# Kernel tuning notes

Hardware: AMD Instinct MI355X
Metric: run time of the kernel (lower is better)

Reference implementation:

```python
import jax, jax.numpy as jnp
import numpy as np

B, N, D, H = 8, 2048, 256, 8
HD = D // H  # head_dim = 32
LN_EPS = 1e-5


def setup_inputs() -> dict:
    key = jax.random.key(0)
    ks = jax.random.split(key, 8)
    x = jax.random.normal(ks[0], (B, N, D), dtype=jnp.float32)
    # dense 0/1 adjacency with guaranteed self-loops (avoids all -inf softmax rows)
    adj = jax.random.randint(ks[1], (B, N, N), 0, 2, dtype=jnp.int32)
    adj = jnp.maximum(adj, jnp.eye(N, dtype=jnp.int32)[None, :, :])
    s = 0.02
    Wq = jax.random.normal(ks[2], (D, D), dtype=jnp.float32) * s
    Wk = jax.random.normal(ks[3], (D, D), dtype=jnp.float32) * s
    Wv = jax.random.normal(ks[4], (D, D), dtype=jnp.float32) * s
    Wo = jax.random.normal(ks[5], (D, D), dtype=jnp.float32) * s
    zeros = jnp.zeros((D,), dtype=jnp.float32)
    return {
        "x": x, "adjacency": adj,
        "Wq": Wq, "bq": zeros, "Wk": Wk, "bk": zeros,
        "Wv": Wv, "bv": zeros, "Wo": Wo, "bo": zeros,
        "gamma": jnp.ones((D,), dtype=jnp.float32), "beta": zeros,
    }


def reference(x, adjacency, Wq, bq, Wk, bk, Wv, bv, Wo, bo, gamma, beta):
    b, n, d = x.shape
    q = (x @ Wq + bq).reshape(b, n, H, HD)
    k = (x @ Wk + bk).reshape(b, n, H, HD)
    v = (x @ Wv + bv).reshape(b, n, H, HD)
    # scores: [B, N(query), M(key), H]
    scores = jnp.einsum('bnhd,bmhd->bnmh', q, k) / jnp.sqrt(jnp.float32(HD))
    mask = (adjacency == 0)[..., None]  # [B,N,M,1] broadcasts over heads
    scores = jnp.where(mask, -jnp.inf, scores)
    weights = jax.nn.softmax(scores, axis=2)  # softmax over key axis m
    # dropout is identity in eval mode
    attended = jnp.einsum('bnmh,bmhd->bnhd', weights, v).reshape(b, n, d)
    out = attended @ Wo + bo
    out = out + x  # residual (output.shape == x.shape since input_dim == output_dim)
    mu = jnp.mean(out, axis=-1, keepdims=True)
    var = jnp.mean(jnp.square(out - mu), axis=-1, keepdims=True)
    return (out - mu) * jax.lax.rsqrt(var + LN_EPS) * gamma + beta
```

## Files before the change

### kernel.cpp

```cpp
#include <hip/hip_runtime.h>
#include <hip/hip_bf16.h>
#include <cstdint>
#include <cstddef>

#define B_ 8
#define N_ 2048
#define D_ 256
#define H_ 8
#define HD_ 32
#define LN_EPS 1e-5f
#define QSCALE 0.25506275f

typedef __attribute__((ext_vector_type(8))) short short8;
typedef __attribute__((ext_vector_type(4))) float f32x4;
typedef __attribute__((ext_vector_type(16))) float f32x16;

static __device__ __forceinline__ float exp2v(float x) {
#if __has_builtin(__builtin_amdgcn_exp2f)
    return __builtin_amdgcn_exp2f(x);
#else
    float r;
    asm("v_exp_f32 %0, %1" : "=v"(r) : "v"(x));
    return r;
#endif
}

static __device__ __forceinline__ unsigned short f2bf(float f) {
    union { float f; unsigned int u; } v; v.f = f;
    unsigned int r = v.u + 0x7fffu + ((v.u >> 16) & 1u);
    return (unsigned short)(r >> 16);
}

static __device__ __forceinline__ unsigned int cvtpk(float lo, float hi) {
    unsigned int d;
    asm("v_cvt_pk_bf16_f32 %0, %1, %2" : "=v"(d) : "v"(lo), "v"(hi));
    return d;
}

__global__ __launch_bounds__(256) void k_prep_w(const float* __restrict__ w0, const float* __restrict__ w1,
                                                const float* __restrict__ w2, const float* __restrict__ w3,
                                                unsigned short* __restrict__ wt) {
    int c = blockIdx.x, mat = blockIdx.y, k = threadIdx.x;
    const float* w = (mat == 0) ? w0 : (mat == 1) ? w1 : (mat == 2) ? w2 : w3;
    wt[((size_t)(mat * 256 + c)) * 256 + k] = f2bf(w[k * 256 + c]);
}

__global__ __launch_bounds__(512) void k_maskF(const int* __restrict__ adj,
                                               unsigned int* __restrict__ mbgT2) {
    __shared__ unsigned int bits[64][66];
    int tid = threadIdx.x, lane = tid & 63, wv = tid >> 6;
    int b = blockIdx.x >> 5, rg = blockIdx.x & 31;

    const int* base = adj + ((size_t)(b * N_ + rg * 64 + wv * 8)) * N_ + lane;
#pragma unroll 1
    for (int i = 0; i < 8; ++i) {
        const int* prow = base + (size_t)i * N_;
#pragma unroll
        for (int half = 0; half < 2; ++half) {
            int v[16];
#pragma unroll
            for (int j = 0; j < 16; ++j)
                v[j] = prow[half * 1024 + j * 64];
            __builtin_amdgcn_sched_barrier(0);
#pragma unroll
            for (int j = 0; j < 16; ++j) {
                unsigned long long m = __ballot(v[j] != 0);
                if (lane == 0)
                    *reinterpret_cast<unsigned long long*>(&bits[wv * 8 + i][half * 32 + 2 * j]) = m;
            }
        }
    }
    __syncthreads();

    int h = lane >> 5, l31 = lane & 31;
    const unsigned int M[5] = {0x0000FFFFu, 0x00FF00FFu, 0x0F0F0F0Fu, 0x33333333u, 0x55555555u};
#pragma unroll
    for (int j = 0; j < 8; ++j) {
        int kw = wv * 8 + j;
        unsigned int w = bits[lane][kw];
#pragma unroll
        for (int si = 0; si < 5; ++si) {
            int s = 16 >> si;
            unsigned int m = M[si];
            unsigned int t = (unsigned int)__shfl_xor((int)w, s, 64);
            unsigned int a = (w & m) | ((t & m) << s);
            unsigned int c = (w & ~m) | ((t >> s) & m);
            w = (lane & s) ? c : a;
        }
        int k = kw * 32 + l31;
        int kp = (k & ~7) | ((k & 3) << 1) | ((k >> 2) & 1);
        mbgT2[((size_t)(b * 64 + rg * 2 + h)) * 2048 + kp] = w;
    }
}

__global__ __launch_bounds__(256) void k_qkv(const float* __restrict__ x,
                                             const unsigned short* __restrict__ wt,
                                             const float* __restrict__ bq, const float* __restrict__ bk,
                                             const float* __restrict__ bv,
                                             unsigned short* __restrict__ Qts, unsigned short* __restrict__ Ks,
                                             unsigned short* __restrict__ Vs) {
    int mat = blockIdx.y;
    int lane = threadIdx.x & 63;
    int wv = threadIdx.x >> 6;
    int row0 = blockIdx.x * 64 + wv * 16;
    int l15 = lane & 15, lg = lane >> 4;
    const float* bias = (mat == 0) ? bq : (mat == 1) ? bk : bv;
    const float qs = (mat == 0) ? QSCALE : 1.0f;
    const unsigned short* wm = wt + (size_t)mat * 65536;

    short8 af[8];
    const float* xrow = x + (size_t)(row0 + l15) * 256 + lg * 8;
#pragma unroll
    for (int kk = 0; kk < 8; ++kk) {
        float4 a = *reinterpret_cast<const float4*>(xrow + kk * 32);
        float4 b = *reinterpret_cast<const float4*>(xrow + kk * 32 + 4);
        union { short8 s8; unsigned int u[4]; } t;
        t.u[0] = cvtpk(a.x, a.y); t.u[1] = cvtpk(a.z, a.w);
        t.u[2] = cvtpk(b.x, b.y); t.u[3] = cvtpk(b.z, b.w);
        af[kk] = t.s8;
    }

    int b = row0 >> 11;
    int nbase = (row0 & 2047) + lg * 4;

    if (mat < 2) {
        unsigned short* dst = (mat == 0) ? Qts : Ks;
        int n = (row0 & 2047) + l15;
        for (int ci = 0; ci < 16; ++ci) {
            const unsigned short* wrow = wm + (size_t)(ci * 16 + l15) * 256 + lg * 8;
            f32x4 acc = {0.f, 0.f, 0.f, 0.f};
#pragma unroll
            for (int kk = 0; kk < 8; ++kk) {
                short8 bfg = *reinterpret_cast<const short8*>(wrow + kk * 32);
                acc = __builtin_amdgcn_mfma_f32_16x16x32_bf16(bfg, af[kk], acc, 0, 0, 0);
            }
            int col0 = ci * 16 + lg * 4;
            float4 b4 = *reinterpret_cast<const float4*>(bias + col0);
            int h = col0 >> 5;
            int hd0 = col0 & 31;
            size_t off = (size_t)(b * 8 + h) * 65536 + (size_t)(n >> 5) * 1024
                       + (size_t)(hd0 >> 4) * 512
                       + (size_t)((((hd0 >> 3) & 1) * 32 + (n & 31))) * 8 + (hd0 & 7);
            ushort4 o;
            o.x = f2bf((acc[0] + b4.x) * qs); o.y = f2bf((acc[1] + b4.y) * qs);
            o.z = f2bf((acc[2] + b4.z) * qs); o.w = f2bf((acc[3] + b4.w) * qs);
            *reinterpret_cast<ushort4*>(dst + off) = o;
        }
    } else {
        for (int ci = 0; ci < 16; ++ci) {
            const unsigned short* wrow = wm + (size_t)(ci * 16 + l15) * 256 + lg * 8;
            f32x4 acc = {0.f, 0.f, 0.f, 0.f};
#pragma unroll
            for (int kk = 0; kk < 8; ++kk) {
                short8 bfg = *reinterpret_cast<const short8*>(wrow + kk * 32);
                acc = __builtin_amdgcn_mfma_f32_16x16x32_bf16(af[kk], bfg, acc, 0, 0, 0);
            }
            int col = ci * 16 + l15;
            float bcol = bias[col];
            int h = col >> 5, hd = col & 31;
            int posb = nbase & 31;
            size_t off = (size_t)(b * 8 + h) * 65536 + (size_t)(nbase >> 5) * 1024
                       + (posb >> 4) * 512 + ((((posb >> 3) & 1) * 32 + hd)) * 8 + (posb & 7);
            ushort4 o;
            o.x = f2bf(acc[0] + bcol); o.y = f2bf(acc[1] + bcol);
            o.z = f2bf(acc[2] + bcol); o.w = f2bf(acc[3] + bcol);
            *reinterpret_cast<ushort4*>(Vs + off) = o;
        }
    }
}

#define SL(j, offs) asm("s_load_dwordx2 %0, %1, " offs : "=s"(m##j) : "s"(mbase))
#define SLOAD16() do { \
    SL(0, "0x0");  SL(1, "0x8");  SL(2, "0x10"); SL(3, "0x18"); \
    SL(4, "0x20"); SL(5, "0x28"); SL(6, "0x30"); SL(7, "0x38"); \
    SL(8, "0x40"); SL(9, "0x48"); SL(10, "0x50"); SL(11, "0x58"); \
    SL(12, "0x60"); SL(13, "0x68"); SL(14, "0x70"); SL(15, "0x78"); } while (0)
#define CND(d, s_, mj) asm("v_cndmask_b32 %0, 0, %1, %2" : "=v"(d) : "v"(s_), "s"(mj))

__global__ __launch_bounds__(256, 5) void k_attn(const unsigned short* __restrict__ Qts,
                                                 const unsigned short* __restrict__ Kb,
                                                 const unsigned short* __restrict__ Vs,
                                                 const unsigned int* __restrict__ mbgT2,
                                                 unsigned short* __restrict__ att) {
    int tid = threadIdx.x;
    int lane = tid & 63;
    int l31 = lane & 31, hi = lane >> 5;
    int b = blockIdx.x & 7;
    int hg = (blockIdx.x >> 3) & 1;
    int qt32 = blockIdx.x >> 4;
    int q0 = qt32 * 32;
    int head = hg * 4 + (tid >> 6);
    int bh = b * 8 + head;

    const unsigned short* Qh = Qts + (size_t)bh * 65536 + (size_t)qt32 * 1024 + (size_t)lane * 8;
    const unsigned short* Kh = Kb + (size_t)bh * 65536;
    const unsigned short* Vh = Vs + (size_t)bh * 65536;

    short8 qf0 = *reinterpret_cast<const short8*>(Qh);
    short8 qf1 = *reinterpret_cast<const short8*>(Qh + 512);
    const unsigned short* krow = Kh + (size_t)lane * 8;
    const unsigned short* vfp = Vh + (size_t)lane * 8;

    unsigned long long mbase = (unsigned long long)(mbgT2 + (size_t)(b * 64 + qt32) * 2048);
    unsigned long long m0, m1, m2, m3, m4, m5, m6, m7, m8, m9, m10, m11, m12, m13, m14, m15;
    SLOAD16();

    const f32x16 fz = {0.f,0.f,0.f,0.f,0.f,0.f,0.f,0.f,0.f,0.f,0.f,0.f,0.f,0.f,0.f,0.f};
    f32x16 attacc = fz;
    float lsum = 0.f;

#pragma unroll 2
    for (int t = 0; t < 64; ++t) {
        short8 kf0 = *reinterpret_cast<const short8*>(krow + (size_t)t * 1024);
        short8 kf1 = *reinterpret_cast<const short8*>(krow + (size_t)t * 1024 + 512);
        short8 vf0 = *reinterpret_cast<const short8*>(vfp + (size_t)t * 1024);
        short8 vf1 = *reinterpret_cast<const short8*>(vfp + (size_t)t * 1024 + 512);

        f32x16 s = __builtin_amdgcn_mfma_f32_32x32x16_bf16(kf0, qf0, fz, 0, 0, 0);
        s = __builtin_amdgcn_mfma_f32_32x32x16_bf16(kf1, qf1, s, 0, 0, 0);

        float e0 = exp2v(s[0]),  e1 = exp2v(s[1]),  e2 = exp2v(s[2]),  e3 = exp2v(s[3]);
        float e4 = exp2v(s[4]),  e5 = exp2v(s[5]),  e6 = exp2v(s[6]),  e7 = exp2v(s[7]);
        float e8 = exp2v(s[8]),  e9 = exp2v(s[9]),  e10 = exp2v(s[10]), e11 = exp2v(s[11]);
        float e12 = exp2v(s[12]), e13 = exp2v(s[13]), e14 = exp2v(s[14]), e15 = exp2v(s[15]);

        asm volatile("s_waitcnt lgkmcnt(0)"
                     : "+s"(m0), "+s"(m1), "+s"(m2), "+s"(m3), "+s"(m4), "+s"(m5), "+s"(m6), "+s"(m7),
                       "+s"(m8), "+s"(m9), "+s"(m10), "+s"(m11), "+s"(m12), "+s"(m13), "+s"(m14), "+s"(m15));

        float p0, p1, p2, p3, p4, p5, p6, p7, p8, p9, p10, p11, p12, p13, p14, p15;
        CND(p0, e0, m0);   CND(p1, e1, m1);   CND(p2, e2, m2);   CND(p3, e3, m3);
        CND(p4, e4, m4);   CND(p5, e5, m5);   CND(p6, e6, m6);   CND(p7, e7, m7);
        CND(p8, e8, m8);   CND(p9, e9, m9);   CND(p10, e10, m10); CND(p11, e11, m11);
        CND(p12, e12, m12); CND(p13, e13, m13); CND(p14, e14, m14); CND(p15, e15, m15);

        lsum += ((p0 + p1) + (p2 + p3)) + ((p4 + p5) + (p6 + p7))
              + ((p8 + p9) + (p10 + p11)) + ((p12 + p13) + (p14 + p15));

        unsigned int pd[4][2];
        pd[0][0] = cvtpk(p0, p1);   pd[0][1] = cvtpk(p2, p3);
        pd[1][0] = cvtpk(p4, p5);   pd[1][1] = cvtpk(p6, p7);
        pd[2][0] = cvtpk(p8, p9);   pd[2][1] = cvtpk(p10, p11);
        pd[3][0] = cvtpk(p12, p13); pd[3][1] = cvtpk(p14, p15);

        mbase += 128;
        SLOAD16();

        asm("v_permlane32_swap_b32 %0, %1" : "+v"(pd[0][0]), "+v"(pd[1][0]));
        asm("v_permlane32_swap_b32 %0, %1" : "+v"(pd[0][1]), "+v"(pd[1][1]));
        asm("v_permlane32_swap_b32 %0, %1" : "+v"(pd[2][0]), "+v"(pd[3][0]));
        asm("v_permlane32_swap_b32 %0, %1" : "+v"(pd[2][1]), "+v"(pd[3][1]));

        union { short8 s8; unsigned int u[4]; } bf0, bf1;
        bf0.u[0] = pd[0][0]; bf0.u[1] = pd[0][1]; bf0.u[2] = pd[1][0]; bf0.u[3] = pd[1][1];
        bf1.u[0] = pd[2][0]; bf1.u[1] = pd[2][1]; bf1.u[2] = pd[3][0]; bf1.u[3] = pd[3][1];

        attacc = __builtin_amdgcn_mfma_f32_32x32x16_bf16(vf0, bf0.s8, attacc, 0, 0, 0);
        attacc = __builtin_amdgcn_mfma_f32_32x32x16_bf16(vf1, bf1.s8, attacc, 0, 0, 0);
    }

    lsum += __shfl_xor(lsum, 32, 64);
    float rcp = 1.f / lsum;

    unsigned short* arow = att + ((size_t)b * N_ + q0 + l31) * D_ + head * HD_;
#pragma unroll
    for (int g = 0; g < 4; ++g) {
        ushort4 o;
        o.x = f2bf(attacc[4 * g + 0] * rcp);
        o.y = f2bf(attacc[4 * g + 1] * rcp);
        o.z = f2bf(attacc[4 * g + 2] * rcp);
        o.w = f2bf(attacc[4 * g + 3] * rcp);
        *reinterpret_cast<ushort4*>(arow + 8 * g + 4 * hi) = o;
    }
}

__global__ __launch_bounds__(256) void k_outln(const unsigned short* __restrict__ att,
                                               const unsigned short* __restrict__ wot,
                                               const float* __restrict__ bo,
                                               const float* __restrict__ x,
                                               const float* __restrict__ gamma, const float* __restrict__ beta,
                                               float* __restrict__ out) {
    int lane = threadIdx.x & 63, wv = threadIdx.x >> 6;
    int l15 = lane & 15, lg = lane >> 4;
    int row0 = blockIdx.x * 64 + wv * 16;
    size_t row = (size_t)(row0 + l15);

    short8 af[8];
    const unsigned short* arow = att + row * 256 + lg * 8;
#pragma unroll
    for (int kk = 0; kk < 8; ++kk)
        af[kk] = *reinterpret_cast<const short8*>(arow + kk * 32);

    float v[16][4];
    float sum = 0.f, sq = 0.f;
#pragma unroll
    for (int ci = 0; ci < 16; ++ci) {
        const unsigned short* wrow = wot + (size_t)(ci * 16 + l15) * 256 + lg * 8;
        f32x4 acc = {0.f, 0.f, 0.f, 0.f};
#pragma unroll
        for (int kk = 0; kk < 8; ++kk) {
            short8 bfg = *reinterpret_cast<const short8*>(wrow + kk * 32);
            acc = __builtin_amdgcn_mfma_f32_16x16x32_bf16(bfg, af[kk], acc, 0, 0, 0);
        }
        int col0 = ci * 16 + lg * 4;
        float4 b4 = *reinterpret_cast<const float4*>(bo + col0);
        float4 x4 = *reinterpret_cast<const float4*>(x + row * 256 + col0);
        v[ci][0] = acc[0] + b4.x + x4.x;
        v[ci][1] = acc[1] + b4.y + x4.y;
        v[ci][2] = acc[2] + b4.z + x4.z;
        v[ci][3] = acc[3] + b4.w + x4.w;
#pragma unroll
        for (int r = 0; r < 4; ++r) {
            sum += v[ci][r];
            sq += v[ci][r] * v[ci][r];
        }
    }

    sum += __shfl_xor(sum, 16, 64); sq += __shfl_xor(sq, 16, 64);
    sum += __shfl_xor(sum, 32, 64); sq += __shfl_xor(sq, 32, 64);

    float mu = sum * (1.f / 256.f);
    float var = sq * (1.f / 256.f) - mu * mu;
    float rs = rsqrtf(var + LN_EPS);

#pragma unroll
    for (int ci = 0; ci < 16; ++ci) {
        int col0 = ci * 16 + lg * 4;
        float4 g4 = *reinterpret_cast<const float4*>(gamma + col0);
        float4 be4 = *reinterpret_cast<const float4*>(beta + col0);
        float4 o;
        o.x = (v[ci][0] - mu) * rs * g4.x + be4.x;
        o.y = (v[ci][1] - mu) * rs * g4.y + be4.y;
        o.z = (v[ci][2] - mu) * rs * g4.z + be4.z;
        o.w = (v[ci][3] - mu) * rs * g4.w + be4.w;
        *reinterpret_cast<float4*>(out + row * 256 + col0) = o;
    }
}

extern "C" void kernel_launch(void* const* d_in, const int* in_sizes, int n_in,
                              void* d_out, int out_size, void* d_ws, size_t ws_size,
                              hipStream_t stream) {
    (void)in_sizes; (void)n_in; (void)out_size; (void)ws_size;
    const float* x     = (const float*)d_in[0];
    const int*   adj   = (const int*)d_in[1];
    const float* Wq    = (const float*)d_in[2];
    const float* bq    = (const float*)d_in[3];
    const float* Wk    = (const float*)d_in[4];
    const float* bk    = (const float*)d_in[5];
    const float* Wv    = (const float*)d_in[6];
    const float* bv    = (const float*)d_in[7];
    const float* Wo    = (const float*)d_in[8];
    const float* bo    = (const float*)d_in[9];
    const float* gamma = (const float*)d_in[10];
    const float* beta  = (const float*)d_in[11];
    float* out = (float*)d_out;

    char* ws = (char*)d_ws;
    unsigned short* wt   = (unsigned short*)ws; ws += (size_t)4 * 256 * 256 * 2;
    unsigned short* Qts  = (unsigned short*)ws; ws += (size_t)B_ * H_ * N_ * HD_ * 2;
    unsigned short* Ks   = (unsigned short*)ws; ws += (size_t)B_ * H_ * N_ * HD_ * 2;
    unsigned short* Vs   = (unsigned short*)ws; ws += (size_t)B_ * H_ * N_ * HD_ * 2;
    unsigned short* att  = (unsigned short*)ws; ws += (size_t)16384 * 256 * 2;
    unsigned int*   mbgT2 = (unsigned int*)ws;  ws += (size_t)B_ * 64 * 2048 * 4 + 8192;

    k_prep_w<<<dim3(256, 4), 256, 0, stream>>>(Wq, Wk, Wv, Wo, wt);
    k_maskF<<<256, 512, 0, stream>>>(adj, mbgT2);
    k_qkv<<<dim3(256, 3), 256, 0, stream>>>(x, wt, bq, bk, bv, Qts, Ks, Vs);
    k_attn<<<1024, 256, 0, stream>>>(Qts, Ks, Vs, mbgT2, att);
    k_outln<<<256, 256, 0, stream>>>(att, wt + 3 * 65536, bo, x, gamma, beta, out);
}
```

Baseline: 176.0 us.

## Process two 32-query tiles per wave to reuse K/V fragments

Each attention wave now handles 64 queries as two 32-row tiles that share the K and V fragments loaded per key step. The grid is halved and the launch-bounds occupancy target drops from 5 to 4. The intent is to halve K/V global traffic per query and to interleave two independent MFMA/exp chains so they hide each other's latency. The cost is more registers (two accumulators, two scalar mask sets), fewer waves per CU, and only 512 blocks, which may underfill the GPU.

```diff
diff --git a/kernel.cpp b/kernel.cpp
--- a/kernel.cpp
+++ b/kernel.cpp
@@ -169,15 +169,21 @@
     }
 }
 
-#define SL(j, offs) asm("s_load_dwordx2 %0, %1, " offs : "=s"(m##j) : "s"(mbase))
-#define SLOAD16() do { \
-    SL(0, "0x0");  SL(1, "0x8");  SL(2, "0x10"); SL(3, "0x18"); \
-    SL(4, "0x20"); SL(5, "0x28"); SL(6, "0x30"); SL(7, "0x38"); \
-    SL(8, "0x40"); SL(9, "0x48"); SL(10, "0x50"); SL(11, "0x58"); \
-    SL(12, "0x60"); SL(13, "0x68"); SL(14, "0x70"); SL(15, "0x78"); } while (0)
+#define SLA(j, offs) asm("s_load_dwordx2 %0, %1, " offs : "=s"(ma##j) : "s"(mbaseA))
+#define SLOADA16() do { \
+    SLA(0, "0x0");  SLA(1, "0x8");  SLA(2, "0x10"); SLA(3, "0x18"); \
+    SLA(4, "0x20"); SLA(5, "0x28"); SLA(6, "0x30"); SLA(7, "0x38"); \
+    SLA(8, "0x40"); SLA(9, "0x48"); SLA(10, "0x50"); SLA(11, "0x58"); \
+    SLA(12, "0x60"); SLA(13, "0x68"); SLA(14, "0x70"); SLA(15, "0x78"); } while (0)
+#define SLB(j, offs) asm("s_load_dwordx2 %0, %1, " offs : "=s"(mb##j) : "s"(mbaseB))
+#define SLOADB16() do { \
+    SLB(0, "0x0");  SLB(1, "0x8");  SLB(2, "0x10"); SLB(3, "0x18"); \
+    SLB(4, "0x20"); SLB(5, "0x28"); SLB(6, "0x30"); SLB(7, "0x38"); \
+    SLB(8, "0x40"); SLB(9, "0x48"); SLB(10, "0x50"); SLB(11, "0x58"); \
+    SLB(12, "0x60"); SLB(13, "0x68"); SLB(14, "0x70"); SLB(15, "0x78"); } while (0)
 #define CND(d, s_, mj) asm("v_cndmask_b32 %0, 0, %1, %2" : "=v"(d) : "v"(s_), "s"(mj))
 
-__global__ __launch_bounds__(256, 5) void k_attn(const unsigned short* __restrict__ Qts,
+__global__ __launch_bounds__(256, 4) void k_attn(const unsigned short* __restrict__ Qts,
                                                  const unsigned short* __restrict__ Kb,
                                                  const unsigned short* __restrict__ Vs,
                                                  const unsigned int* __restrict__ mbgT2,
@@ -187,90 +193,144 @@
     int l31 = lane & 31, hi = lane >> 5;
     int b = blockIdx.x & 7;
     int hg = (blockIdx.x >> 3) & 1;
-    int qt32 = blockIdx.x >> 4;
-    int q0 = qt32 * 32;
+    int qt64 = blockIdx.x >> 4;
+    int qtA = qt64 * 2;
     int head = hg * 4 + (tid >> 6);
     int bh = b * 8 + head;
 
-    const unsigned short* Qh = Qts + (size_t)bh * 65536 + (size_t)qt32 * 1024 + (size_t)lane * 8;
+    const unsigned short* QhA = Qts + (size_t)bh * 65536 + (size_t)qtA * 1024 + (size_t)lane * 8;
     const unsigned short* Kh = Kb + (size_t)bh * 65536;
     const unsigned short* Vh = Vs + (size_t)bh * 65536;
 
-    short8 qf0 = *reinterpret_cast<const short8*>(Qh);
-    short8 qf1 = *reinterpret_cast<const short8*>(Qh + 512);
+    short8 qfA0 = *reinterpret_cast<const short8*>(QhA);
+    short8 qfA1 = *reinterpret_cast<const short8*>(QhA + 512);
+    short8 qfB0 = *reinterpret_cast<const short8*>(QhA + 1024);
+    short8 qfB1 = *reinterpret_cast<const short8*>(QhA + 1536);
     const unsigned short* krow = Kh + (size_t)lane * 8;
     const unsigned short* vfp = Vh + (size_t)lane * 8;
 
-    unsigned long long mbase = (unsigned long long)(mbgT2 + (size_t)(b * 64 + qt32) * 2048);
-    unsigned long long m0, m1, m2, m3, m4, m5, m6, m7, m8, m9, m10, m11, m12, m13, m14, m15;
-    SLOAD16();
+    unsigned long long mbaseA = (unsigned long long)(mbgT2 + (size_t)(b * 64 + qtA) * 2048);
+    unsigned long long mbaseB = mbaseA + 8192;
+    unsigned long long ma0, ma1, ma2, ma3, ma4, ma5, ma6, ma7, ma8, ma9, ma10, ma11, ma12, ma13, ma14, ma15;
+    unsigned long long mb0, mb1, mb2, mb3, mb4, mb5, mb6, mb7, mb8, mb9, mb10, mb11, mb12, mb13, mb14, mb15;
+    SLOADA16();
+    SLOADB16();
 
     const f32x16 fz = {0.f,0.f,0.f,0.f,0.f,0.f,0.f,0.f,0.f,0.f,0.f,0.f,0.f,0.f,0.f,0.f};
-    f32x16 attacc = fz;
-    float lsum = 0.f;
-
-#pragma unroll 2
+    f32x16 attaccA = fz, attaccB = fz;
+    float lsumA = 0.f, lsumB = 0.f;
+
+#pragma unroll 1
     for (int t = 0; t < 64; ++t) {
         short8 kf0 = *reinterpret_cast<const short8*>(krow + (size_t)t * 1024);
         short8 kf1 = *reinterpret_cast<const short8*>(krow + (size_t)t * 1024 + 512);
         short8 vf0 = *reinterpret_cast<const short8*>(vfp + (size_t)t * 1024);
         short8 vf1 = *reinterpret_cast<const short8*>(vfp + (size_t)t * 1024 + 512);
 
-        f32x16 s = __builtin_amdgcn_mfma_f32_32x32x16_bf16(kf0, qf0, fz, 0, 0, 0);
-        s = __builtin_amdgcn_mfma_f32_32x32x16_bf16(kf1, qf1, s, 0, 0, 0);
-
-        float e0 = exp2v(s[0]),  e1 = exp2v(s[1]),  e2 = exp2v(s[2]),  e3 = exp2v(s[3]);
-        float e4 = exp2v(s[4]),  e5 = exp2v(s[5]),  e6 = exp2v(s[6]),  e7 = exp2v(s[7]);
-        float e8 = exp2v(s[8]),  e9 = exp2v(s[9]),  e10 = exp2v(s[10]), e11 = exp2v(s[11]);
-        float e12 = exp2v(s[12]), e13 = exp2v(s[13]), e14 = exp2v(s[14]), e15 = exp2v(s[15]);
-
-        asm volatile("s_waitcnt lgkmcnt(0)"
-                     : "+s"(m0), "+s"(m1), "+s"(m2), "+s"(m3), "+s"(m4), "+s"(m5), "+s"(m6), "+s"(m7),
-                       "+s"(m8), "+s"(m9), "+s"(m10), "+s"(m11), "+s"(m12), "+s"(m13), "+s"(m14), "+s"(m15));
-
-        float p0, p1, p2, p3, p4, p5, p6, p7, p8, p9, p10, p11, p12, p13, p14, p15;
-        CND(p0, e0, m0);   CND(p1, e1, m1);   CND(p2, e2, m2);   CND(p3, e3, m3);
-        CND(p4, e4, m4);   CND(p5, e5, m5);   CND(p6, e6, m6);   CND(p7, e7, m7);
-        CND(p8, e8, m8);   CND(p9, e9, m9);   CND(p10, e10, m10); CND(p11, e11, m11);
-        CND(p12, e12, m12); CND(p13, e13, m13); CND(p14, e14, m14); CND(p15, e15, m15);
-
-        lsum += ((p0 + p1) + (p2 + p3)) + ((p4 + p5) + (p6 + p7))
-              + ((p8 + p9) + (p10 + p11)) + ((p12 + p13) + (p14 + p15));
-
-        unsigned int pd[4][2];
-        pd[0][0] = cvtpk(p0, p1);   pd[0][1] = cvtpk(p2, p3);
-        pd[1][0] = cvtpk(p4, p5);   pd[1][1] = cvtpk(p6, p7);
-        pd[2][0] = cvtpk(p8, p9);   pd[2][1] = cvtpk(p10, p11);
-        pd[3][0] = cvtpk(p12, p13); pd[3][1] = cvtpk(p14, p15);
-
-        mbase += 128;
-        SLOAD16();
-
-        asm("v_permlane32_swap_b32 %0, %1" : "+v"(pd[0][0]), "+v"(pd[1][0]));
-        asm("v_permlane32_swap_b32 %0, %1" : "+v"(pd[0][1]), "+v"(pd[1][1]));
-        asm("v_permlane32_swap_b32 %0, %1" : "+v"(pd[2][0]), "+v"(pd[3][0]));
-        asm("v_permlane32_swap_b32 %0, %1" : "+v"(pd[2][1]), "+v"(pd[3][1]));
-
-        union { short8 s8; unsigned int u[4]; } bf0, bf1;
-        bf0.u[0] = pd[0][0]; bf0.u[1] = pd[0][1]; bf0.u[2] = pd[1][0]; bf0.u[3] = pd[1][1];
-        bf1.u[0] = pd[2][0]; bf1.u[1] = pd[2][1]; bf1.u[2] = pd[3][0]; bf1.u[3] = pd[3][1];
-
-        attacc = __builtin_amdgcn_mfma_f32_32x32x16_bf16(vf0, bf0.s8, attacc, 0, 0, 0);
-        attacc = __builtin_amdgcn_mfma_f32_32x32x16_bf16(vf1, bf1.s8, attacc, 0, 0, 0);
-    }
-
-    lsum += __shfl_xor(lsum, 32, 64);
-    float rcp = 1.f / lsum;
-
-    unsigned short* arow = att + ((size_t)b * N_ + q0 + l31) * D_ + head * HD_;
+        f32x16 sA = __builtin_amdgcn_mfma_f32_32x32x16_bf16(kf0, qfA0, fz, 0, 0, 0);
+        sA = __builtin_amdgcn_mfma_f32_32x32x16_bf16(kf1, qfA1, sA, 0, 0, 0);
+        f32x16 sB = __builtin_amdgcn_mfma_f32_32x32x16_bf16(kf0, qfB0, fz, 0, 0, 0);
+        sB = __builtin_amdgcn_mfma_f32_32x32x16_bf16(kf1, qfB1, sB, 0, 0, 0);
+
+        {
+            float e0 = exp2v(sA[0]),  e1 = exp2v(sA[1]),  e2 = exp2v(sA[2]),  e3 = exp2v(sA[3]);
+            float e4 = exp2v(sA[4]),  e5 = exp2v(sA[5]),  e6 = exp2v(sA[6]),  e7 = exp2v(sA[7]);
+            float e8 = exp2v(sA[8]),  e9 = exp2v(sA[9]),  e10 = exp2v(sA[10]), e11 = exp2v(sA[11]);
+            float e12 = exp2v(sA[12]), e13 = exp2v(sA[13]), e14 = exp2v(sA[14]), e15 = exp2v(sA[15]);
+
+            asm volatile("s_waitcnt lgkmcnt(0)"
+                         : "+s"(ma0), "+s"(ma1), "+s"(ma2), "+s"(ma3), "+s"(ma4), "+s"(ma5), "+s"(ma6), "+s"(ma7),
+                           "+s"(ma8), "+s"(ma9), "+s"(ma10), "+s"(ma11), "+s"(ma12), "+s"(ma13), "+s"(ma14), "+s"(ma15));
+
+            float p0, p1, p2, p3, p4, p5, p6, p7, p8, p9, p10, p11, p12, p13, p14, p15;
+            CND(p0, e0, ma0);   CND(p1, e1, ma1);   CND(p2, e2, ma2);   CND(p3, e3, ma3);
+            CND(p4, e4, ma4);   CND(p5, e5, ma5);   CND(p6, e6, ma6);   CND(p7, e7, ma7);
+            CND(p8, e8, ma8);   CND(p9, e9, ma9);   CND(p10, e10, ma10); CND(p11, e11, ma11);
+            CND(p12, e12, ma12); CND(p13, e13, ma13); CND(p14, e14, ma14); CND(p15, e15, ma15);
+
+            lsumA += ((p0 + p1) + (p2 + p3)) + ((p4 + p5) + (p6 + p7))
+                   + ((p8 + p9) + (p10 + p11)) + ((p12 + p13) + (p14 + p15));
+
+            unsigned int pd[4][2];
+            pd[0][0] = cvtpk(p0, p1);   pd[0][1] = cvtpk(p2, p3);
+            pd[1][0] = cvtpk(p4, p5);   pd[1][1] = cvtpk(p6, p7);
+            pd[2][0] = cvtpk(p8, p9);   pd[2][1] = cvtpk(p10, p11);
+            pd[3][0] = cvtpk(p12, p13); pd[3][1] = cvtpk(p14, p15);
+
+            mbaseA += 128;
+            SLOADA16();
+
+            asm("v_permlane32_swap_b32 %0, %1" : "+v"(pd[0][0]), "+v"(pd[1][0]));
+            asm("v_permlane32_swap_b32 %0, %1" : "+v"(pd[0][1]), "+v"(pd[1][1]));
+            asm("v_permlane32_swap_b32 %0, %1" : "+v"(pd[2][0]), "+v"(pd[3][0]));
+            asm("v_permlane32_swap_b32 %0, %1" : "+v"(pd[2][1]), "+v"(pd[3][1]));
+
+            union { short8 s8; unsigned int u[4]; } bf0, bf1;
+            bf0.u[0] = pd[0][0]; bf0.u[1] = pd[0][1]; bf0.u[2] = pd[1][0]; bf0.u[3] = pd[1][1];
+            bf1.u[0] = pd[2][0]; bf1.u[1] = pd[2][1]; bf1.u[2] = pd[3][0]; bf1.u[3] = pd[3][1];
+
+            attaccA = __builtin_amdgcn_mfma_f32_32x32x16_bf16(vf0, bf0.s8, attaccA, 0, 0, 0);
+            attaccA = __builtin_amdgcn_mfma_f32_32x32x16_bf16(vf1, bf1.s8, attaccA, 0, 0, 0);
+        }
+
+        {
+            float e0 = exp2v(sB[0]),  e1 = exp2v(sB[1]),  e2 = exp2v(sB[2]),  e3 = exp2v(sB[3]);
+            float e4 = exp2v(sB[4]),  e5 = exp2v(sB[5]),  e6 = exp2v(sB[6]),  e7 = exp2v(sB[7]);
+            float e8 = exp2v(sB[8]),  e9 = exp2v(sB[9]),  e10 = exp2v(sB[10]), e11 = exp2v(sB[11]);
+            float e12 = exp2v(sB[12]), e13 = exp2v(sB[13]), e14 = exp2v(sB[14]), e15 = exp2v(sB[15]);
+
+            float p0, p1, p2, p3, p4, p5, p6, p7, p8, p9, p10, p11, p12, p13, p14, p15;
+            CND(p0, e0, mb0);   CND(p1, e1, mb1);   CND(p2, e2, mb2);   CND(p3, e3, mb3);
+            CND(p4, e4, mb4);   CND(p5, e5, mb5);   CND(p6, e6, mb6);   CND(p7, e7, mb7);
+            CND(p8, e8, mb8);   CND(p9, e9, mb9);   CND(p10, e10, mb10); CND(p11, e11, mb11);
+            CND(p12, e12, mb12); CND(p13, e13, mb13); CND(p14, e14, mb14); CND(p15, e15, mb15);
+
+            lsumB += ((p0 + p1) + (p2 + p3)) + ((p4 + p5) + (p6 + p7))
+                   + ((p8 + p9) + (p10 + p11)) + ((p12 + p13) + (p14 + p15));
+
+            unsigned int pd[4][2];
+            pd[0][0] = cvtpk(p0, p1);   pd[0][1] = cvtpk(p2, p3);
+            pd[1][0] = cvtpk(p4, p5);   pd[1][1] = cvtpk(p6, p7);
+            pd[2][0] = cvtpk(p8, p9);   pd[2][1] = cvtpk(p10, p11);
+            pd[3][0] = cvtpk(p12, p13); pd[3][1] = cvtpk(p14, p15);
+
+            mbaseB += 128;
+            SLOADB16();
+
+            asm("v_permlane32_swap_b32 %0, %1" : "+v"(pd[0][0]), "+v"(pd[1][0]));
+            asm("v_permlane32_swap_b32 %0, %1" : "+v"(pd[0][1]), "+v"(pd[1][1]));
+            asm("v_permlane32_swap_b32 %0, %1" : "+v"(pd[2][0]), "+v"(pd[3][0]));
+            asm("v_permlane32_swap_b32 %0, %1" : "+v"(pd[2][1]), "+v"(pd[3][1]));
+
+            union { short8 s8; unsigned int u[4]; } bf0, bf1;
+            bf0.u[0] = pd[0][0]; bf0.u[1] = pd[0][1]; bf0.u[2] = pd[1][0]; bf0.u[3] = pd[1][1];
+            bf1.u[0] = pd[2][0]; bf1.u[1] = pd[2][1]; bf1.u[2] = pd[3][0]; bf1.u[3] = pd[3][1];
+
+            attaccB = __builtin_amdgcn_mfma_f32_32x32x16_bf16(vf0, bf0.s8, attaccB, 0, 0, 0);
+            attaccB = __builtin_amdgcn_mfma_f32_32x32x16_bf16(vf1, bf1.s8, attaccB, 0, 0, 0);
+        }
+    }
+
+    lsumA += __shfl_xor(lsumA, 32, 64);
+    lsumB += __shfl_xor(lsumB, 32, 64);
+    float rcpA = 1.f / lsumA;
+    float rcpB = 1.f / lsumB;
+
+    unsigned short* arowA = att + ((size_t)b * N_ + qtA * 32 + l31) * D_ + head * HD_;
+    unsigned short* arowB = arowA + 32 * D_;
 #pragma unroll
     for (int g = 0; g < 4; ++g) {
-        ushort4 o;
-        o.x = f2bf(attacc[4 * g + 0] * rcp);
-        o.y = f2bf(attacc[4 * g + 1] * rcp);
-        o.z = f2bf(attacc[4 * g + 2] * rcp);
-        o.w = f2bf(attacc[4 * g + 3] * rcp);
-        *reinterpret_cast<ushort4*>(arow + 8 * g + 4 * hi) = o;
+        ushort4 oA, oB;
+        oA.x = f2bf(attaccA[4 * g + 0] * rcpA);
+        oA.y = f2bf(attaccA[4 * g + 1] * rcpA);
+        oA.z = f2bf(attaccA[4 * g + 2] * rcpA);
+        oA.w = f2bf(attaccA[4 * g + 3] * rcpA);
+        oB.x = f2bf(attaccB[4 * g + 0] * rcpB);
+        oB.y = f2bf(attaccB[4 * g + 1] * rcpB);
+        oB.z = f2bf(attaccB[4 * g + 2] * rcpB);
+        oB.w = f2bf(attaccB[4 * g + 3] * rcpB);
+        *reinterpret_cast<ushort4*>(arowA + 8 * g + 4 * hi) = oA;
+        *reinterpret_cast<ushort4*>(arowB + 8 * g + 4 * hi) = oB;
     }
 }
 
@@ -361,11 +421,11 @@
     unsigned short* Ks   = (unsigned short*)ws; ws += (size_t)B_ * H_ * N_ * HD_ * 2;
     unsigned short* Vs   = (unsigned short*)ws; ws += (size_t)B_ * H_ * N_ * HD_ * 2;
     unsigned short* att  = (unsigned short*)ws; ws += (size_t)16384 * 256 * 2;
-    unsigned int*   mbgT2 = (unsigned int*)ws;  ws += (size_t)B_ * 64 * 2048 * 4 + 8192;
+    unsigned int*   mbgT2 = (unsigned int*)ws;  ws += (size_t)B_ * 64 * 2048 * 4 + 16384;
 
     k_prep_w<<<dim3(256, 4), 256, 0, stream>>>(Wq, Wk, Wv, Wo, wt);
     k_maskF<<<256, 512, 0, stream>>>(adj, mbgT2);
     k_qkv<<<dim3(256, 3), 256, 0, stream>>>(x, wt, bq, bk, bv, Qts, Ks, Vs);
-    k_attn<<<1024, 256, 0, stream>>>(Qts, Ks, Vs, mbgT2, att);
+    k_attn<<<512, 256, 0, stream>>>(Qts, Ks, Vs, mbgT2, att);
     k_outln<<<256, 256, 0, stream>>>(att, wt + 3 * 65536, bo, x, gamma, beta, out);
 }
```

Result: slower. 209.5 us (+19.1%).
